# Kernel optimization log

Measured on AMD Instinct MI355X. Metric: run time of the kernel, lower is better.

Reference implementation:

```python
import jax, jax.numpy as jnp
import numpy as np

EPS = 1e-5
N_NODES = 100000
C_IN = 128
C_OUT = 128
N_EDGES = 3200000


def setup_inputs() -> dict:
    key = jax.random.key(0)
    k1, k2, k3 = jax.random.split(key, 3)
    x = jax.random.normal(k1, (N_NODES, C_IN), dtype=jnp.float32)
    edge_index = jax.random.randint(k2, (2, N_EDGES), 0, N_NODES, dtype=jnp.int64)
    # BatchNorm1d affine params
    gamma = jnp.ones((C_IN,), dtype=jnp.float32)
    beta = jnp.zeros((C_IN,), dtype=jnp.float32)
    # GCNConv linear weight (glorot) and bias
    limit = np.sqrt(6.0 / (C_IN + C_OUT)).astype(np.float32)
    W = jax.random.uniform(k3, (C_IN, C_OUT), minval=-limit, maxval=limit, dtype=jnp.float32)
    b = jnp.zeros((C_OUT,), dtype=jnp.float32)
    return {"x": x, "edge_index": edge_index, "gamma": gamma, "beta": beta, "W": W, "b": b}


def reference(x, edge_index, gamma, beta, W, b):
    n = x.shape[0]
    # --- BatchNorm1d (training mode: batch statistics, biased variance) ---
    mean = jnp.mean(x, axis=0)
    var = jnp.mean(jnp.square(x - mean), axis=0)
    xn = (x - mean) * jax.lax.rsqrt(var + EPS) * gamma + beta
    # --- GCNConv: linear, add self-loops, symmetric normalization, scatter-add ---
    h = xn @ W  # [n, C_out]
    loops = jnp.arange(n, dtype=edge_index.dtype)
    row = jnp.concatenate([edge_index[0], loops])  # source nodes
    col = jnp.concatenate([edge_index[1], loops])  # target nodes
    deg = jax.ops.segment_sum(jnp.ones_like(col, dtype=h.dtype), col, num_segments=n)
    dis = jnp.where(deg > 0, jax.lax.rsqrt(jnp.maximum(deg, 1.0)), 0.0)
    norm = dis[row] * dis[col]  # [E+n]
    msg = h[row] * norm[:, None]  # gather + scale
    out = jax.ops.segment_sum(msg, col, num_segments=n) + b  # scatter-add
    return jax.nn.relu(out)
```

## Files before the change

### kernel.cpp

```cpp
#include <hip/hip_runtime.h>

#define EPS_BN 1e-5f
#define C 128
#define CG 32
#define CAP 6144
#define NBLK 256

typedef __attribute__((ext_vector_type(8))) short bf16x8;
typedef __attribute__((ext_vector_type(4))) float f32x4;

__device__ inline unsigned bf16_rne(float f) {
  unsigned u = __float_as_uint(f);
  return (u + 0x7FFFu + ((u >> 16) & 1u)) >> 16;
}
__device__ inline float bf16_f(unsigned h) { return __uint_as_float(h << 16); }

__global__ void k_init(float* __restrict__ sums) {
  int i = blockIdx.x * blockDim.x + threadIdx.x;
  if (i < 256) sums[i] = 0.0f;
}

__global__ void k_stats(const float4* __restrict__ x4, float* __restrict__ sums, int n) {
  __shared__ float4 s_s[256];
  __shared__ float4 s_q[256];
  int t = threadIdx.x;
  int cg = t & 31;
  int rl = t >> 5;
  float4 s = make_float4(0.f, 0.f, 0.f, 0.f);
  float4 q = make_float4(0.f, 0.f, 0.f, 0.f);
  for (int r = blockIdx.x * 8 + rl; r < n; r += gridDim.x * 8) {
    float4 v = x4[(size_t)r * CG + cg];
    s.x += v.x; s.y += v.y; s.z += v.z; s.w += v.w;
    q.x += v.x * v.x; q.y += v.y * v.y; q.z += v.z * v.z; q.w += v.w * v.w;
  }
  s_s[t] = s; s_q[t] = q;
  __syncthreads();
  if (t < 32) {
    for (int j = 1; j < 8; ++j) {
      float4 a = s_s[t + 32 * j];
      float4 b = s_q[t + 32 * j];
      s.x += a.x; s.y += a.y; s.z += a.z; s.w += a.w;
      q.x += b.x; q.y += b.y; q.z += b.z; q.w += b.w;
    }
    atomicAdd(&sums[t * 4 + 0], s.x);
    atomicAdd(&sums[t * 4 + 1], s.y);
    atomicAdd(&sums[t * 4 + 2], s.z);
    atomicAdd(&sums[t * 4 + 3], s.w);
    atomicAdd(&sums[C + t * 4 + 0], q.x);
    atomicAdd(&sums[C + t * 4 + 1], q.y);
    atomicAdd(&sums[C + t * 4 + 2], q.z);
    atomicAdd(&sums[C + t * 4 + 3], q.w);
  }
}

__global__ void k_finalize(const float* __restrict__ sums,
                           const float* __restrict__ gamma,
                           const float* __restrict__ beta,
                           float* __restrict__ scale, float* __restrict__ shift,
                           int n) {
  int c = threadIdx.x;
  if (c < C) {
    float inv_n = 1.0f / (float)n;
    float mean = sums[c] * inv_n;
    float var = sums[C + c] * inv_n - mean * mean;
    float rstd = rsqrtf(var + EPS_BN);
    float sc = gamma[c] * rstd;
    scale[c] = sc;
    shift[c] = beta[c] - mean * sc;
  }
}

__global__ void k_hist(const int* __restrict__ col, int* __restrict__ histG,
                       int E, int NB, int chunk) {
  __shared__ int h[800];
  int b = blockIdx.x, t = threadIdx.x;
  for (int i = t; i < NB; i += 256) h[i] = 0;
  __syncthreads();
  int s = b * chunk, eend = min(E, s + chunk);
  for (int e = s + t; e < eend; e += 256) atomicAdd(&h[col[e] >> 7], 1);
  __syncthreads();
  for (int i = t; i < NB; i += 256) histG[b * NB + i] = h[i];
}

__global__ void k_scanH(int* __restrict__ histG, int* __restrict__ btot, int NB) {
  __shared__ int sh[NBLK];
  int q = blockIdx.x, t = threadIdx.x;
  int v = histG[t * NB + q];
  sh[t] = v;
  __syncthreads();
  for (int off = 1; off < NBLK; off <<= 1) {
    int a = (t >= off) ? sh[t - off] : 0;
    __syncthreads();
    sh[t] += a;
    __syncthreads();
  }
  histG[t * NB + q] = sh[t] - v;
  if (t == NBLK - 1) btot[q] = sh[t];
}

__global__ void k_scanB(const int* __restrict__ btot, int* __restrict__ boffs,
                        int NB, int E) {
  __shared__ int sh[1024];
  int t = threadIdx.x;
  int v = (t < NB) ? btot[t] : 0;
  sh[t] = v;
  __syncthreads();
  for (int off = 1; off < 1024; off <<= 1) {
    int a = (t >= off) ? sh[t - off] : 0;
    __syncthreads();
    sh[t] += a;
    __syncthreads();
  }
  if (t < NB) boffs[t] = sh[t] - v;
  if (t == 0) boffs[NB] = E;
}

__global__ void k_part(const int* __restrict__ row, const int* __restrict__ col,
                       const int* __restrict__ histG, const int* __restrict__ boffs,
                       unsigned* __restrict__ binned, int E, int NB, int chunk) {
  __shared__ int cur[800];
  int b = blockIdx.x, t = threadIdx.x;
  for (int i = t; i < NB; i += 256) cur[i] = boffs[i] + histG[b * NB + i];
  __syncthreads();
  int s = b * chunk, eend = min(E, s + chunk);
  for (int e = s + t; e < eend; e += 256) {
    int c = col[e];
    int pos = atomicAdd(&cur[c >> 7], 1);
    binned[pos] = ((unsigned)(c & 127) << 17) | (unsigned)row[e];
  }
}

__global__ __launch_bounds__(256) void k_reorder(
    unsigned* __restrict__ binned, const int* __restrict__ boffs,
    int* __restrict__ noffs, float* __restrict__ dis, int n, int E) {
  __shared__ int cnt[128];
  __shared__ int offs[128];
  __shared__ int cur[128];
  __shared__ int scn[128];
  __shared__ unsigned list[CAP];
  int b = blockIdx.x, t = threadIdx.x;
  if (t < 128) cnt[t] = 0;
  __syncthreads();
  int s = boffs[b], e = boffs[b + 1];
  for (int i = s + t; i < e; i += 256) atomicAdd(&cnt[binned[i] >> 17], 1);
  __syncthreads();
  if (t < 128) scn[t] = cnt[t];
  __syncthreads();
  for (int off = 1; off < 128; off <<= 1) {
    int a = (t >= off && t < 128) ? scn[t - off] : 0;
    __syncthreads();
    if (t < 128) scn[t] += a;
    __syncthreads();
  }
  if (t < 128) {
    offs[t] = scn[t] - cnt[t];
    cur[t] = scn[t] - cnt[t];
  }
  __syncthreads();
  for (int i = s + t; i < e; i += 256) {
    unsigned v = binned[i];
    int pos = atomicAdd(&cur[v >> 17], 1);
    if (pos < CAP) list[pos] = v & 0x1FFFFu;
  }
  __syncthreads();
  int len = e - s;
  for (int i = t; i < len; i += 256) binned[s + i] = list[i];
  int node = b * 128 + t;
  if (t < 128 && node < n) {
    noffs[node] = s + offs[t];
    dis[node] = rsqrtf((float)(cnt[t] + 1));
  }
  if (b == 0 && t == 0) noffs[n] = E;
}

__global__ void k_prep(const float2* __restrict__ x2, const float* __restrict__ dis,
                       const float2* __restrict__ scale2,
                       const float2* __restrict__ shift2,
                       unsigned* __restrict__ y, int n) {
  int idx = blockIdx.x * blockDim.x + threadIdx.x;
  int r = idx >> 6;
  if (r >= n) return;
  int lane = idx & 63;
  float d = dis[r];
  float2 v = x2[(size_t)r * 64 + lane];
  float2 sc = scale2[lane], sh = shift2[lane];
  float y0 = (v.x * sc.x + sh.x) * d;
  float y1 = (v.y * sc.y + sh.y) * d;
  y[(size_t)r * 64 + lane] = (bf16_rne(y1) << 16) | bf16_rne(y0);
}

__global__ __launch_bounds__(256) void k_G2(
    const unsigned* __restrict__ y, const unsigned* __restrict__ lst,
    const int* __restrict__ noffs, const float* __restrict__ dis,
    unsigned* __restrict__ ghi, unsigned* __restrict__ glo, int n) {
  int w = (blockIdx.x * blockDim.x + threadIdx.x) >> 6;
  if (w >= n) return;
  int lane = threadIdx.x & 63;
  int h = lane >> 5;
  int q = lane & 31;
  int s = noffs[w], t = noffs[w + 1];
  float4 a0 = make_float4(0.f, 0.f, 0.f, 0.f);
  float4 a1 = make_float4(0.f, 0.f, 0.f, 0.f);
  float4 a2 = make_float4(0.f, 0.f, 0.f, 0.f);
  float4 a3 = make_float4(0.f, 0.f, 0.f, 0.f);
  int i = s;
  for (; i + 7 < t; i += 8) {
    int r0 = lst[i + h],     r1 = lst[i + 2 + h];
    int r2 = lst[i + 4 + h], r3 = lst[i + 6 + h];
    uint2 u0 = *(const uint2*)(y + (size_t)r0 * 64 + q * 2);
    uint2 u1 = *(const uint2*)(y + (size_t)r1 * 64 + q * 2);
    uint2 u2 = *(const uint2*)(y + (size_t)r2 * 64 + q * 2);
    uint2 u3 = *(const uint2*)(y + (size_t)r3 * 64 + q * 2);
    a0.x += __uint_as_float(u0.x << 16); a0.y += __uint_as_float(u0.x & 0xFFFF0000u);
    a0.z += __uint_as_float(u0.y << 16); a0.w += __uint_as_float(u0.y & 0xFFFF0000u);
    a1.x += __uint_as_float(u1.x << 16); a1.y += __uint_as_float(u1.x & 0xFFFF0000u);
    a1.z += __uint_as_float(u1.y << 16); a1.w += __uint_as_float(u1.y & 0xFFFF0000u);
    a2.x += __uint_as_float(u2.x << 16); a2.y += __uint_as_float(u2.x & 0xFFFF0000u);
    a2.z += __uint_as_float(u2.y << 16); a2.w += __uint_as_float(u2.y & 0xFFFF0000u);
    a3.x += __uint_as_float(u3.x << 16); a3.y += __uint_as_float(u3.x & 0xFFFF0000u);
    a3.z += __uint_as_float(u3.y << 16); a3.w += __uint_as_float(u3.y & 0xFFFF0000u);
  }
  for (int j = i + h; j < t; j += 2) {
    uint2 u = *(const uint2*)(y + (size_t)lst[j] * 64 + q * 2);
    a0.x += __uint_as_float(u.x << 16); a0.y += __uint_as_float(u.x & 0xFFFF0000u);
    a0.z += __uint_as_float(u.y << 16); a0.w += __uint_as_float(u.y & 0xFFFF0000u);
  }
  if (h == 0) {
    uint2 u = *(const uint2*)(y + (size_t)w * 64 + q * 2);
    a0.x += __uint_as_float(u.x << 16); a0.y += __uint_as_float(u.x & 0xFFFF0000u);
    a0.z += __uint_as_float(u.y << 16); a0.w += __uint_as_float(u.y & 0xFFFF0000u);
  }
  float vx = a0.x + a1.x + a2.x + a3.x;
  float vy = a0.y + a1.y + a2.y + a3.y;
  float vz = a0.z + a1.z + a2.z + a3.z;
  float vw = a0.w + a1.w + a2.w + a3.w;
  vx += __shfl_xor(vx, 32);
  vy += __shfl_xor(vy, 32);
  vz += __shfl_xor(vz, 32);
  vw += __shfl_xor(vw, 32);
  if (h == 0) {
    float dc = dis[w];
    float g0 = dc * vx, g1 = dc * vy, g2 = dc * vz, g3 = dc * vw;
    unsigned h0 = bf16_rne(g0), h1 = bf16_rne(g1);
    unsigned h2 = bf16_rne(g2), h3 = bf16_rne(g3);
    unsigned l0 = bf16_rne(g0 - bf16_f(h0)), l1 = bf16_rne(g1 - bf16_f(h1));
    unsigned l2 = bf16_rne(g2 - bf16_f(h2)), l3 = bf16_rne(g3 - bf16_f(h3));
    uint2 hw, lw;
    hw.x = (h1 << 16) | h0; hw.y = (h3 << 16) | h2;
    lw.x = (l1 << 16) | l0; lw.y = (l3 << 16) | l2;
    *(uint2*)(ghi + (size_t)w * 64 + q * 2) = hw;
    *(uint2*)(glo + (size_t)w * 64 + q * 2) = lw;
  }
}

__global__ __launch_bounds__(256) void k_gemmM(
    const unsigned* __restrict__ ghi, const unsigned* __restrict__ glo,
    const float* __restrict__ W, const float* __restrict__ bias,
    float* __restrict__ out, int n) {
  __shared__ __align__(16) unsigned short sGh[64][136];
  __shared__ __align__(16) unsigned short sGl[64][136];
  __shared__ __align__(16) unsigned short sWt[128][136];
  int t = threadIdx.x;
  int rowBase = blockIdx.x * 64;
  for (int i = t; i < 16384; i += 256) {
    int k = i >> 7, c = i & 127;
    sWt[c][k] = (unsigned short)bf16_rne(W[i]);
  }
  for (int i = t; i < 4096; i += 256) {
    int r = i >> 6, c = i & 63;
    int rw = rowBase + r;
    unsigned uh = 0, ul = 0;
    if (rw < n) {
      uh = ghi[(size_t)rw * 64 + c];
      ul = glo[(size_t)rw * 64 + c];
    }
    *(unsigned*)&sGh[r][c * 2] = uh;
    *(unsigned*)&sGl[r][c * 2] = ul;
  }
  __syncthreads();
  int w = t >> 6, l = t & 63;
  int m16 = l & 15, kb = l >> 4;
  int rtile = w * 16;
  f32x4 acc[8];
#pragma unroll
  for (int i = 0; i < 8; ++i) acc[i] = (f32x4){0.f, 0.f, 0.f, 0.f};
#pragma unroll
  for (int kt = 0; kt < 4; ++kt) {
    int koff = kt * 32 + kb * 8;
    bf16x8 ah = *(const bf16x8*)&sGh[rtile + m16][koff];
    bf16x8 al = *(const bf16x8*)&sGl[rtile + m16][koff];
#pragma unroll
    for (int nt = 0; nt < 8; ++nt) {
      bf16x8 bb = *(const bf16x8*)&sWt[nt * 16 + m16][koff];
      acc[nt] = __builtin_amdgcn_mfma_f32_16x16x32_bf16(ah, bb, acc[nt], 0, 0, 0);
      acc[nt] = __builtin_amdgcn_mfma_f32_16x16x32_bf16(al, bb, acc[nt], 0, 0, 0);
    }
  }
#pragma unroll
  for (int nt = 0; nt < 8; ++nt) {
    int colc = nt * 16 + m16;
    float bv = bias[colc];
#pragma unroll
    for (int reg = 0; reg < 4; ++reg) {
      int row = rowBase + rtile + kb * 4 + reg;
      if (row < n) {
        float o = acc[nt][reg] + bv;
        out[(size_t)row * C + colc] = fmaxf(o, 0.f);
      }
    }
  }
}

__global__ __launch_bounds__(256) void k_G(
    const unsigned* __restrict__ y, const unsigned* __restrict__ lst,
    const int* __restrict__ noffs, const float* __restrict__ dis,
    const float2* __restrict__ x2, const float2* __restrict__ scale2,
    const float2* __restrict__ shift2, float2* __restrict__ out2,
    int n, int useY) {
  int w = (blockIdx.x * blockDim.x + threadIdx.x) >> 6;
  if (w >= n) return;
  int lane = threadIdx.x & 63;
  int s = noffs[w], t = noffs[w + 1];
  float2 a0 = make_float2(0.f, 0.f), a1 = make_float2(0.f, 0.f);
  float2 a2 = make_float2(0.f, 0.f), a3 = make_float2(0.f, 0.f);
  if (useY) {
    int i = s;
    for (; i + 3 < t; i += 4) {
      int r0 = lst[i], r1 = lst[i + 1], r2 = lst[i + 2], r3 = lst[i + 3];
      unsigned u0 = y[(size_t)r0 * 64 + lane];
      unsigned u1 = y[(size_t)r1 * 64 + lane];
      unsigned u2 = y[(size_t)r2 * 64 + lane];
      unsigned u3 = y[(size_t)r3 * 64 + lane];
      a0.x += __uint_as_float(u0 << 16); a0.y += __uint_as_float(u0 & 0xFFFF0000u);
      a1.x += __uint_as_float(u1 << 16); a1.y += __uint_as_float(u1 & 0xFFFF0000u);
      a2.x += __uint_as_float(u2 << 16); a2.y += __uint_as_float(u2 & 0xFFFF0000u);
      a3.x += __uint_as_float(u3 << 16); a3.y += __uint_as_float(u3 & 0xFFFF0000u);
    }
    for (; i < t; ++i) {
      unsigned u = y[(size_t)lst[i] * 64 + lane];
      a0.x += __uint_as_float(u << 16); a0.y += __uint_as_float(u & 0xFFFF0000u);
    }
    float dc = dis[w];
    float2 o;
    o.x = dc * (a0.x + a1.x + a2.x + a3.x);
    o.y = dc * (a0.y + a1.y + a2.y + a3.y);
    out2[(size_t)w * 64 + lane] = o;
  } else {
    float sd = 0.f;
    for (int i = s; i < t; ++i) {
      int r = lst[i];
      float d = dis[r];
      float2 v = x2[(size_t)r * 64 + lane];
      a0.x += v.x * d; a0.y += v.y * d; sd += d;
    }
    float dc = dis[w];
    float2 sc = scale2[lane], sh = shift2[lane];
    float2 o;
    o.x = dc * (a0.x * sc.x + sd * sh.x);
    o.y = dc * (a0.y * sc.y + sd * sh.y);
    out2[(size_t)w * 64 + lane] = o;
  }
}

__global__ __launch_bounds__(256) void k_gemm(float* __restrict__ out,
                        const float4* __restrict__ x4,
                        const float* __restrict__ W,
                        const float* __restrict__ bias,
                        const float* __restrict__ scale,
                        const float* __restrict__ shift,
                        const float* __restrict__ dis, int n) {
  __shared__ float sW[64 * C];
  __shared__ float sG[32 * C];
  int t = threadIdx.x;
  int rowBase = blockIdx.x * 32;

  const float4* scale4 = (const float4*)scale;
  const float4* shift4 = (const float4*)shift;
  float4* sG4 = (float4*)sG;
  float4* sW4 = (float4*)sW;
  const float4* W4 = (const float4*)W;
  const float4* out4 = (const float4*)out;

  for (int i = t; i < 32 * CG; i += 256) {
    int r = i >> 5, g = i & 31;
    int rw = rowBase + r;
    float4 acc = make_float4(0.f, 0.f, 0.f, 0.f);
    if (rw < n) {
      acc = out4[(size_t)rw * CG + g];
      float4 xv = x4[(size_t)rw * CG + g];
      float d = dis[rw];
      float inv = d * d;
      float4 sc = scale4[g];
      float4 sh = shift4[g];
      acc.x += (xv.x * sc.x + sh.x) * inv;
      acc.y += (xv.y * sc.y + sh.y) * inv;
      acc.z += (xv.z * sc.z + sh.z) * inv;
      acc.w += (xv.w * sc.w + sh.w) * inv;
    }
    sG4[i] = acc;
  }

  int tx = t & 127;
  int ty = t >> 7;
  float acc[16];
#pragma unroll
  for (int i = 0; i < 16; ++i) acc[i] = 0.f;

  for (int kc = 0; kc < 2; ++kc) {
    for (int i = t; i < 64 * C / 4; i += 256) sW4[i] = W4[kc * 2048 + i];
    __syncthreads();
#pragma unroll 4
    for (int k = 0; k < 64; ++k) {
      float w = sW[k * C + tx];
#pragma unroll
      for (int rr = 0; rr < 16; ++rr)
        acc[rr] += sG[(rr * 2 + ty) * C + kc * 64 + k] * w;
    }
    __syncthreads();
  }

  float bv = bias[tx];
#pragma unroll
  for (int rr = 0; rr < 16; ++rr) {
    int rw = rowBase + rr * 2 + ty;
    if (rw < n) {
      float o = acc[rr] + bv;
      out[(size_t)rw * C + tx] = o > 0.f ? o : 0.f;
    }
  }
}

extern "C" void kernel_launch(void* const* d_in, const int* in_sizes, int n_in,
                              void* d_out, int out_size, void* d_ws, size_t ws_size,
                              hipStream_t stream) {
  const float* x = (const float*)d_in[0];
  const int* edge = (const int*)d_in[1];
  const float* gamma = (const float*)d_in[2];
  const float* beta = (const float*)d_in[3];
  const float* W = (const float*)d_in[4];
  const float* bias = (const float*)d_in[5];
  float* out = (float*)d_out;

  int n = in_sizes[0] / C;
  int E = in_sizes[1] / 2;
  int NB = (n + 127) / 128;
  int chunk = (E + NBLK - 1) / NBLK;

  float* ws = (float*)d_ws;
  float* sums = ws;
  float* scale = ws + 256;
  float* shift = ws + 384;
  float* dis = ws + 512;
  int* btot = (int*)(ws + 512 + n);
  int* boffs = btot + NB;
  int* noffs = boffs + NB + 1;
  int* histG = noffs + n + 1;
  unsigned* binned = (unsigned*)(histG + (size_t)NBLK * NB);
  unsigned* y = binned + E;
  unsigned* ghi = y + (size_t)n * 64;
  unsigned* glo = ghi + (size_t)n * 64;

  size_t base = (size_t)512 + n + NB + (NB + 1) + (n + 1) +
                (size_t)NBLK * NB + E;
  size_t need_old = base + (size_t)n * 64;
  size_t need_new = base + (size_t)n * 64 * 3;
  int mode = (ws_size >= need_new * 4) ? 2 : (ws_size >= need_old * 4) ? 1 : 0;

  k_init<<<1, 256, 0, stream>>>(sums);
  k_stats<<<256, 256, 0, stream>>>((const float4*)x, sums, n);
  k_finalize<<<1, 128, 0, stream>>>(sums, gamma, beta, scale, shift, n);
  k_hist<<<NBLK, 256, 0, stream>>>(edge + E, histG, E, NB, chunk);
  k_scanH<<<NB, NBLK, 0, stream>>>(histG, btot, NB);
  k_scanB<<<1, 1024, 0, stream>>>(btot, boffs, NB, E);
  k_part<<<NBLK, 256, 0, stream>>>(edge, edge + E, histG, boffs, binned, E, NB, chunk);
  k_reorder<<<NB, 256, 0, stream>>>(binned, boffs, noffs, dis, n, E);
  if (mode >= 1) {
    k_prep<<<(n * 64 + 255) / 256, 256, 0, stream>>>(
        (const float2*)x, dis, (const float2*)scale, (const float2*)shift, y, n);
  }
  if (mode == 2) {
    k_G2<<<(n * 64 + 255) / 256, 256, 0, stream>>>(y, binned, noffs, dis,
                                                   ghi, glo, n);
    k_gemmM<<<(n + 63) / 64, 256, 0, stream>>>(ghi, glo, W, bias, out, n);
  } else {
    k_G<<<(n * 64 + 255) / 256, 256, 0, stream>>>(
        y, binned, noffs, dis, (const float2*)x, (const float2*)scale,
        (const float2*)shift, (float2*)out, n, mode);
    k_gemm<<<(n + 31) / 32, 256, 0, stream>>>(out, (const float4*)x, W, bias,
                                              scale, shift, dis, n);
  }
}
```

Baseline: 346.0 us.

## Precompute bf16 W transpose, per-wave reorder counters, larger hist/part blocks

Adds a tiny kernel that converts and transposes W to bf16 once, so each GEMM block loads it with vector copies instead of converting 16K floats per block. k_reorder splits its shared-memory counters per wavefront to reduce atomic contention. k_hist and k_part move to 512-thread blocks, and k_stats gets more blocks for parallelism. The costs are an extra kernel launch and a little more workspace, and k_stats correctness depends on how it strides over rows.

```diff
diff --git a/kernel.cpp b/kernel.cpp
--- a/kernel.cpp
+++ b/kernel.cpp
@@ -70,16 +70,17 @@
   }
 }
 
-__global__ void k_hist(const int* __restrict__ col, int* __restrict__ histG,
-                       int E, int NB, int chunk) {
+__global__ __launch_bounds__(512) void k_hist(const int* __restrict__ col,
+                                              int* __restrict__ histG,
+                                              int E, int NB, int chunk) {
   __shared__ int h[800];
   int b = blockIdx.x, t = threadIdx.x;
-  for (int i = t; i < NB; i += 256) h[i] = 0;
+  for (int i = t; i < NB; i += 512) h[i] = 0;
   __syncthreads();
   int s = b * chunk, eend = min(E, s + chunk);
-  for (int e = s + t; e < eend; e += 256) atomicAdd(&h[col[e] >> 7], 1);
-  __syncthreads();
-  for (int i = t; i < NB; i += 256) histG[b * NB + i] = h[i];
+  for (int e = s + t; e < eend; e += 512) atomicAdd(&h[col[e] >> 7], 1);
+  __syncthreads();
+  for (int i = t; i < NB; i += 512) histG[b * NB + i] = h[i];
 }
 
 __global__ void k_scanH(int* __restrict__ histG, int* __restrict__ btot, int NB) {
@@ -115,15 +116,16 @@
   if (t == 0) boffs[NB] = E;
 }
 
-__global__ void k_part(const int* __restrict__ row, const int* __restrict__ col,
+__global__ __launch_bounds__(512) void k_part(const int* __restrict__ row,
+                       const int* __restrict__ col,
                        const int* __restrict__ histG, const int* __restrict__ boffs,
                        unsigned* __restrict__ binned, int E, int NB, int chunk) {
   __shared__ int cur[800];
   int b = blockIdx.x, t = threadIdx.x;
-  for (int i = t; i < NB; i += 256) cur[i] = boffs[i] + histG[b * NB + i];
+  for (int i = t; i < NB; i += 512) cur[i] = boffs[i] + histG[b * NB + i];
   __syncthreads();
   int s = b * chunk, eend = min(E, s + chunk);
-  for (int e = s + t; e < eend; e += 256) {
+  for (int e = s + t; e < eend; e += 512) {
     int c = col[e];
     int pos = atomicAdd(&cur[c >> 7], 1);
     binned[pos] = ((unsigned)(c & 127) << 17) | (unsigned)row[e];
@@ -133,18 +135,23 @@
 __global__ __launch_bounds__(256) void k_reorder(
     unsigned* __restrict__ binned, const int* __restrict__ boffs,
     int* __restrict__ noffs, float* __restrict__ dis, int n, int E) {
+  __shared__ int cnt4[4][128];
+  __shared__ int cur4[4][128];
   __shared__ int cnt[128];
   __shared__ int offs[128];
-  __shared__ int cur[128];
   __shared__ int scn[128];
   __shared__ unsigned list[CAP];
   int b = blockIdx.x, t = threadIdx.x;
-  if (t < 128) cnt[t] = 0;
+  int w = t >> 6;
+  for (int i = t; i < 512; i += 256) ((int*)cnt4)[i] = 0;
   __syncthreads();
   int s = boffs[b], e = boffs[b + 1];
-  for (int i = s + t; i < e; i += 256) atomicAdd(&cnt[binned[i] >> 17], 1);
-  __syncthreads();
-  if (t < 128) scn[t] = cnt[t];
+  for (int i = s + t; i < e; i += 256) atomicAdd(&cnt4[w][binned[i] >> 17], 1);
+  __syncthreads();
+  if (t < 128) {
+    cnt[t] = cnt4[0][t] + cnt4[1][t] + cnt4[2][t] + cnt4[3][t];
+    scn[t] = cnt[t];
+  }
   __syncthreads();
   for (int off = 1; off < 128; off <<= 1) {
     int a = (t >= off && t < 128) ? scn[t - off] : 0;
@@ -153,13 +160,17 @@
     __syncthreads();
   }
   if (t < 128) {
-    offs[t] = scn[t] - cnt[t];
-    cur[t] = scn[t] - cnt[t];
+    int o = scn[t] - cnt[t];
+    offs[t] = o;
+    cur4[0][t] = o;
+    cur4[1][t] = o + cnt4[0][t];
+    cur4[2][t] = o + cnt4[0][t] + cnt4[1][t];
+    cur4[3][t] = o + cnt4[0][t] + cnt4[1][t] + cnt4[2][t];
   }
   __syncthreads();
   for (int i = s + t; i < e; i += 256) {
     unsigned v = binned[i];
-    int pos = atomicAdd(&cur[v >> 17], 1);
+    int pos = atomicAdd(&cur4[w][v >> 17], 1);
     if (pos < CAP) list[pos] = v & 0x1FFFFu;
   }
   __syncthreads();
@@ -187,6 +198,14 @@
   float y0 = (v.x * sc.x + sh.x) * d;
   float y1 = (v.y * sc.y + sh.y) * d;
   y[(size_t)r * 64 + lane] = (bf16_rne(y1) << 16) | bf16_rne(y0);
+}
+
+__global__ void k_wt(const float* __restrict__ W, unsigned short* __restrict__ Wt) {
+  int i = blockIdx.x * 256 + threadIdx.x;
+  if (i < C * C) {
+    int k = i >> 7, c = i & 127;
+    Wt[c * C + k] = (unsigned short)bf16_rne(W[i]);
+  }
 }
 
 __global__ __launch_bounds__(256) void k_G2(
@@ -255,16 +274,16 @@
 
 __global__ __launch_bounds__(256) void k_gemmM(
     const unsigned* __restrict__ ghi, const unsigned* __restrict__ glo,
-    const float* __restrict__ W, const float* __restrict__ bias,
+    const unsigned short* __restrict__ Wt, const float* __restrict__ bias,
     float* __restrict__ out, int n) {
   __shared__ __align__(16) unsigned short sGh[64][136];
   __shared__ __align__(16) unsigned short sGl[64][136];
   __shared__ __align__(16) unsigned short sWt[128][136];
   int t = threadIdx.x;
   int rowBase = blockIdx.x * 64;
-  for (int i = t; i < 16384; i += 256) {
-    int k = i >> 7, c = i & 127;
-    sWt[c][k] = (unsigned short)bf16_rne(W[i]);
+  for (int i = t; i < 2048; i += 256) {
+    int c = i >> 4, kq = i & 15;
+    *(uint4*)&sWt[c][kq * 8] = *(const uint4*)(Wt + c * C + kq * 8);
   }
   for (int i = t; i < 4096; i += 256) {
     int r = i >> 6, c = i & 63;
@@ -459,29 +478,32 @@
   unsigned* y = binned + E;
   unsigned* ghi = y + (size_t)n * 64;
   unsigned* glo = ghi + (size_t)n * 64;
+  unsigned short* Wt = (unsigned short*)(((uintptr_t)(glo + (size_t)n * 64) + 15) &
+                                         ~(uintptr_t)15);
 
   size_t base = (size_t)512 + n + NB + (NB + 1) + (n + 1) +
                 (size_t)NBLK * NB + E;
   size_t need_old = base + (size_t)n * 64;
-  size_t need_new = base + (size_t)n * 64 * 3;
+  size_t need_new = base + (size_t)n * 64 * 3 + 2048 + 8;
   int mode = (ws_size >= need_new * 4) ? 2 : (ws_size >= need_old * 4) ? 1 : 0;
 
   k_init<<<1, 256, 0, stream>>>(sums);
-  k_stats<<<256, 256, 0, stream>>>((const float4*)x, sums, n);
+  k_stats<<<1024, 256, 0, stream>>>((const float4*)x, sums, n);
   k_finalize<<<1, 128, 0, stream>>>(sums, gamma, beta, scale, shift, n);
-  k_hist<<<NBLK, 256, 0, stream>>>(edge + E, histG, E, NB, chunk);
+  k_hist<<<NBLK, 512, 0, stream>>>(edge + E, histG, E, NB, chunk);
   k_scanH<<<NB, NBLK, 0, stream>>>(histG, btot, NB);
   k_scanB<<<1, 1024, 0, stream>>>(btot, boffs, NB, E);
-  k_part<<<NBLK, 256, 0, stream>>>(edge, edge + E, histG, boffs, binned, E, NB, chunk);
+  k_part<<<NBLK, 512, 0, stream>>>(edge, edge + E, histG, boffs, binned, E, NB, chunk);
   k_reorder<<<NB, 256, 0, stream>>>(binned, boffs, noffs, dis, n, E);
   if (mode >= 1) {
     k_prep<<<(n * 64 + 255) / 256, 256, 0, stream>>>(
         (const float2*)x, dis, (const float2*)scale, (const float2*)shift, y, n);
   }
   if (mode == 2) {
+    k_wt<<<(C * C + 255) / 256, 256, 0, stream>>>(W, Wt);
     k_G2<<<(n * 64 + 255) / 256, 256, 0, stream>>>(y, binned, noffs, dis,
                                                    ghi, glo, n);
-    k_gemmM<<<(n + 63) / 64, 256, 0, stream>>>(ghi, glo, W, bias, out, n);
+    k_gemmM<<<(n + 63) / 64, 256, 0, stream>>>(ghi, glo, Wt, bias, out, n);
   } else {
     k_G<<<(n * 64 + 255) / 256, 256, 0, stream>>>(
         y, binned, noffs, dis, (const float2*)x, (const float2*)scale,
```

After: 393.9 us. 13.9% more time.
